# Kernel tuning notes

Measured on AMD Instinct MI355X. Metric: run time of the kernel, lower is better.

The kernel has to match this reference:

```python
import jax, jax.numpy as jnp
import numpy as np

NUM_SELECTS = 2
NOISE_EPS = 0.01
LOSS_COEF = 0.01
INV_SQRT2 = 0.7071067811865476


def _phi(z):
    # standard normal CDF
    return 0.5 * (1.0 + jax.lax.erf(z * INV_SQRT2))


def _cv_squared(v, eps=1e-10):
    # torch .var() uses unbiased estimator (ddof=1)
    return jnp.var(v, ddof=1) / (jnp.mean(v) ** 2 + eps)


def setup_inputs() -> dict:
    key = jax.random.key(0)
    ks = jax.random.split(key, 5)
    T, D, E = 8192, 4096, 16
    return {
        "x": jax.random.normal(ks[0], (T, D), jnp.float32),
        "gate_w1": jax.random.normal(ks[1], (E, D), jnp.float32) * 0.02,
        "gate_w2": jax.random.normal(ks[2], (E, E), jnp.float32) * 0.02,
        "noise_w": jax.random.normal(ks[3], (E, D), jnp.float32) * 0.02,
        "noise": jax.random.normal(ks[4], (T, E), jnp.float32),
    }


def reference(x, gate_w1, gate_w2, noise_w, noise):
    T = x.shape[0]
    # gate network: Linear -> tanh -> Linear (no biases)
    logits_gate = jnp.tanh(x @ gate_w1.T) @ gate_w2.T          # [T, E]
    noise_control = jax.nn.softplus(x @ noise_w.T) + NOISE_EPS  # [T, E]
    logits_noise = noise * noise_control                        # [T, E]
    logits = logits_gate + logits_noise

    # top (k+1) for load-balancing thresholds
    top_logits, top_indices = jax.lax.top_k(logits, NUM_SELECTS + 1)
    top_k_logits = top_logits[:, :NUM_SELECTS]
    top_k_indices = top_indices[:, :NUM_SELECTS]
    top_k_scores = jax.nn.softmax(top_k_logits, axis=1)

    # importance: scatter top-k scores back to [T, E]
    rows = jnp.arange(T)[:, None]
    scores_filtered = jnp.zeros_like(logits).at[rows, top_k_indices].set(top_k_scores)
    importance = scores_filtered.sum(0)  # [E]

    # load: prob each expert would be in the top-k under the noise model
    thr_in = top_logits[:, NUM_SELECTS][:, None]        # (k+1)-th largest
    thr_out = top_logits[:, NUM_SELECTS - 1][:, None]   # k-th largest
    is_in = logits_noise > thr_in
    prob_if_in = _phi((logits_gate - thr_in) / noise_control)
    prob_if_out = _phi((logits_gate - thr_out) / noise_control)
    load = jnp.where(is_in, prob_if_in, prob_if_out).sum(0)  # [E]

    gate_loss = (_cv_squared(importance) + _cv_squared(load)) * LOSS_COEF
    return top_k_indices, top_k_scores, gate_loss
```

## Files before the change

kernel.cpp:

```cpp
#include <hip/hip_runtime.h>
#include <math.h>

#define TT 8192
#define DD 4096

typedef float  f32x4  __attribute__((ext_vector_type(4)));
typedef short  bf16x8 __attribute__((ext_vector_type(8)));
typedef unsigned int u32;
typedef unsigned short u16;

__global__ __launch_bounds__(128)
void split_w(const float* __restrict__ gw1, const float* __restrict__ nw,
             u32* __restrict__ wfrag, float* __restrict__ iml) {
  const int s = blockIdx.x;
  const int t = threadIdx.x;
  if (s == 0 && t < 32) iml[t] = 0.f;
  const int h = t >> 6, l = t & 63;
  const int e = h * 16 + (l & 15);
  const float* src = ((e < 16) ? (gw1 + (size_t)e * DD) : (nw + (size_t)(e - 16) * DD))
                     + s * 32 + ((l >> 4) << 3);
  float f[8];
  *(float4*)&f[0] = *(const float4*)src;
  *(float4*)&f[4] = *(const float4*)(src + 4);
  u32 u0[8], u1[8], u2[8];
#pragma unroll
  for (int i = 0; i < 8; ++i) {
    u0[i] = __float_as_uint(f[i]);
    const float r1 = f[i] - __uint_as_float(u0[i] & 0xFFFF0000u);
    u1[i] = __float_as_uint(r1);
    const float r2 = r1 - __uint_as_float(u1[i] & 0xFFFF0000u);
    u2[i] = __float_as_uint(r2);
  }
  const size_t base = ((size_t)s * 2 + h) * 256 + l * 4;
#define PK(U) make_uint4((U[0]>>16)|(U[1]&0xFFFF0000u), (U[2]>>16)|(U[3]&0xFFFF0000u), \
                         (U[4]>>16)|(U[5]&0xFFFF0000u), (U[6]>>16)|(U[7]&0xFFFF0000u))
  *(uint4*)(wfrag + base)                 = PK(u0);
  *(uint4*)(wfrag + base + 128 * 512)     = PK(u1);
  *(uint4*)(wfrag + base + 2 * 128 * 512) = PK(u2);
#undef PK
}

__global__ __launch_bounds__(256)
void gate_gemm(const float* __restrict__ x, const u32* __restrict__ wfrag,
               float* __restrict__ part) {
  const int t = threadIdx.x;
  const int wt = blockIdx.x * 4 + (t >> 6);
  const int l = t & 63;
  const int rt = wt >> 3;
  const int ksl = wt & 7;
  const int r = l & 15, c = l >> 4;
  const float* xp = x + (size_t)(rt * 16 + r) * DD + ksl * 512 + (c << 3);
  const u32* wfl = wfrag + (size_t)l * 4;

  f32x4 ag0 = {0,0,0,0}, ag1 = ag0, ag2 = ag0, an0 = ag0, an1 = ag0, an2 = ag0;

#pragma unroll 4
  for (int sl = 0; sl < 16; ++sl) {
    float f[8];
    *(float4*)&f[0] = *(const float4*)(xp + sl * 32);
    *(float4*)&f[4] = *(const float4*)(xp + sl * 32 + 4);

    const int S = ksl * 16 + sl;
    const u32* wb = wfl + (size_t)S * 512;
    const bf16x8 bg0 = *(const bf16x8*)(wb);
    const bf16x8 bn0 = *(const bf16x8*)(wb + 256);
    const bf16x8 bg1 = *(const bf16x8*)(wb + 128 * 512);
    const bf16x8 bn1 = *(const bf16x8*)(wb + 128 * 512 + 256);
    const bf16x8 bg2 = *(const bf16x8*)(wb + 2 * 128 * 512);
    const bf16x8 bn2 = *(const bf16x8*)(wb + 2 * 128 * 512 + 256);

    u32 u0[8], u1[8], u2[8];
#pragma unroll
    for (int i = 0; i < 8; ++i) {
      u0[i] = __float_as_uint(f[i]);
      const float r1 = f[i] - __uint_as_float(u0[i] & 0xFFFF0000u);
      u1[i] = __float_as_uint(r1);
      const float r2 = r1 - __uint_as_float(u1[i] & 0xFFFF0000u);
      u2[i] = __float_as_uint(r2);
    }
    u32 pk[12];
#pragma unroll
    for (int i = 0; i < 4; ++i) {
      pk[i]     = (u0[2*i] >> 16) | (u0[2*i+1] & 0xFFFF0000u);
      pk[4 + i] = (u1[2*i] >> 16) | (u1[2*i+1] & 0xFFFF0000u);
      pk[8 + i] = (u2[2*i] >> 16) | (u2[2*i+1] & 0xFFFF0000u);
    }
    const bf16x8 a0 = *(const bf16x8*)&pk[0];
    const bf16x8 a1 = *(const bf16x8*)&pk[4];
    const bf16x8 a2 = *(const bf16x8*)&pk[8];

    ag0 = __builtin_amdgcn_mfma_f32_16x16x32_bf16(a0, bg0, ag0, 0, 0, 0);
    an0 = __builtin_amdgcn_mfma_f32_16x16x32_bf16(a0, bn0, an0, 0, 0, 0);
    ag1 = __builtin_amdgcn_mfma_f32_16x16x32_bf16(a0, bg1, ag1, 0, 0, 0);
    an1 = __builtin_amdgcn_mfma_f32_16x16x32_bf16(a0, bn1, an1, 0, 0, 0);
    ag2 = __builtin_amdgcn_mfma_f32_16x16x32_bf16(a1, bg0, ag2, 0, 0, 0);
    an2 = __builtin_amdgcn_mfma_f32_16x16x32_bf16(a1, bn0, an2, 0, 0, 0);
    ag0 = __builtin_amdgcn_mfma_f32_16x16x32_bf16(a0, bg2, ag0, 0, 0, 0);
    an0 = __builtin_amdgcn_mfma_f32_16x16x32_bf16(a0, bn2, an0, 0, 0, 0);
    ag1 = __builtin_amdgcn_mfma_f32_16x16x32_bf16(a1, bg1, ag1, 0, 0, 0);
    an1 = __builtin_amdgcn_mfma_f32_16x16x32_bf16(a1, bn1, an1, 0, 0, 0);
    ag2 = __builtin_amdgcn_mfma_f32_16x16x32_bf16(a2, bg0, ag2, 0, 0, 0);
    an2 = __builtin_amdgcn_mfma_f32_16x16x32_bf16(a2, bn0, an2, 0, 0, 0);
  }

  const f32x4 cg = ag0 + ag1 + ag2;
  const f32x4 cn = an0 + an1 + an2;
  const int e = l & 15;
  const int rbase = rt * 16 + ((l >> 4) << 2);
  *(f32x4*)&part[((size_t)(ksl * 32 + e)) * TT + rbase]      = cg;
  *(f32x4*)&part[((size_t)(ksl * 32 + 16 + e)) * TT + rbase] = cn;
}

__global__ __launch_bounds__(256)
void gate_epilogue(const float* __restrict__ part, const float* __restrict__ noise,
                   const float* __restrict__ gw2, float* __restrict__ out,
                   float* __restrict__ iml) {
  const int row = blockIdx.x * 256 + threadIdx.x;
  float dot[32];
#pragma unroll
  for (int e = 0; e < 32; ++e) {
    float s = 0.f;
#pragma unroll
    for (int sl = 0; sl < 8; ++sl) s += part[((size_t)(sl * 32 + e)) * TT + row];
    dot[e] = s;
  }
  float h[16];
#pragma unroll
  for (int e = 0; e < 16; ++e) h[e] = tanhf(dot[e]);
  float lg[16], nc[16], ln[16], l[16];
#pragma unroll
  for (int j = 0; j < 16; ++j) {
    float s = 0.f;
#pragma unroll
    for (int e = 0; e < 16; ++e) s = fmaf(h[e], gw2[j * 16 + e], s);
    lg[j] = s;
    const float v = dot[16 + j];
    nc[j] = fmaxf(v, 0.f) + log1pf(expf(-fabsf(v))) + 0.01f;
    ln[j] = noise[(size_t)row * 16 + j] * nc[j];
    l[j] = lg[j] + ln[j];
  }
  int i0 = 0; float m0 = l[0];
#pragma unroll
  for (int j = 1; j < 16; ++j) if (l[j] > m0) { m0 = l[j]; i0 = j; }
  int i1 = -1; float m1 = -1e30f;
#pragma unroll
  for (int j = 0; j < 16; ++j) if (j != i0 && l[j] > m1) { m1 = l[j]; i1 = j; }
  float m2 = -1e30f;
#pragma unroll
  for (int j = 0; j < 16; ++j) if (j != i0 && j != i1 && l[j] > m2) m2 = l[j];

  const float e1 = expf(m1 - m0);
  const float s0 = 1.f / (1.f + e1);
  const float s1 = e1 / (1.f + e1);
  out[(size_t)row * 2]             = (float)i0;
  out[(size_t)row * 2 + 1]         = (float)i1;
  out[16384 + (size_t)row * 2]     = s0;
  out[16384 + (size_t)row * 2 + 1] = s1;

  float c[32];
#pragma unroll
  for (int j = 0; j < 16; ++j) {
    c[j] = (j == i0) ? s0 : ((j == i1) ? s1 : 0.f);
    const bool in = ln[j] > m2;
    const float thr = in ? m2 : m1;
    const float z = (lg[j] - thr) / nc[j];
    c[16 + j] = 0.5f * (1.f + erff(z * 0.70710678118654752f));
  }
#pragma unroll
  for (int off = 32; off; off >>= 1) {
#pragma unroll
    for (int k = 0; k < 32; ++k) c[k] += __shfl_xor(c[k], off, 64);
  }
  __shared__ float sacc[32];
  if (threadIdx.x < 32) sacc[threadIdx.x] = 0.f;
  __syncthreads();
  if ((threadIdx.x & 63) == 0) {
#pragma unroll
    for (int k = 0; k < 32; ++k) atomicAdd(&sacc[k], c[k]);
  }
  __syncthreads();
  if (threadIdx.x < 32) atomicAdd(&iml[threadIdx.x], sacc[threadIdx.x]);
}

__global__ void gate_loss_k(const float* __restrict__ iml, float* __restrict__ out) {
  if (threadIdx.x == 0 && blockIdx.x == 0) {
    float res = 0.f;
    for (int g = 0; g < 2; ++g) {
      const float* v = iml + g * 16;
      float mu = 0.f;
      for (int j = 0; j < 16; ++j) mu += v[j];
      mu *= (1.f / 16.f);
      float var = 0.f;
      for (int j = 0; j < 16; ++j) { const float d = v[j] - mu; var += d * d; }
      var *= (1.f / 15.f);
      res += var / (mu * mu + 1e-10f);
    }
    out[32768] = res * 0.01f;
  }
}

extern "C" void kernel_launch(void* const* d_in, const int* in_sizes, int n_in,
                              void* d_out, int out_size, void* d_ws, size_t ws_size,
                              hipStream_t stream) {
  const float* x     = (const float*)d_in[0];
  const float* gw1   = (const float*)d_in[1];
  const float* gw2   = (const float*)d_in[2];
  const float* nw    = (const float*)d_in[3];
  const float* noise = (const float*)d_in[4];
  float* out  = (float*)d_out;
  float* part = (float*)d_ws;
  u32*   wfrag = (u32*)((char*)d_ws + (size_t)8 * 32 * TT * 4);
  float* iml  = (float*)((char*)d_ws + (size_t)8 * 32 * TT * 4 + (size_t)3 * 128 * 2 * 64 * 16);
  split_w<<<128, 128, 0, stream>>>(gw1, nw, wfrag, iml);
  gate_gemm<<<1024, 256, 0, stream>>>(x, wfrag, part);
  gate_epilogue<<<32, 256, 0, stream>>>(part, noise, gw2, out, iml);
  gate_loss_k<<<1, 64, 0, stream>>>(iml, out);
}
```

Measured before the change: 66.11 us.

## Fuse gate GEMM with epilogue and reduce partial sums in shared memory

Merges the split-K GEMM and the epilogue into one kernel. Each 512-thread block handles 16 rows with 8 waves, one per K slice, and sums the partials in LDS instead of writing an 8x32xT partial buffer to global memory and reading it back. Per-block importance and load sums go to a small buffer that the final loss kernel reduces deterministically, so the global atomics and the zeroing of iml in split_w are no longer needed. In exchange, only 16 of 512 threads run the epilogue math, which serialises that tail work inside each block.

```diff
diff --git a/kernel.cpp b/kernel.cpp
--- a/kernel.cpp
+++ b/kernel.cpp
@@ -7,14 +7,12 @@
 typedef float  f32x4  __attribute__((ext_vector_type(4)));
 typedef short  bf16x8 __attribute__((ext_vector_type(8)));
 typedef unsigned int u32;
-typedef unsigned short u16;
 
 __global__ __launch_bounds__(128)
 void split_w(const float* __restrict__ gw1, const float* __restrict__ nw,
-             u32* __restrict__ wfrag, float* __restrict__ iml) {
+             u32* __restrict__ wfrag) {
   const int s = blockIdx.x;
   const int t = threadIdx.x;
-  if (s == 0 && t < 32) iml[t] = 0.f;
   const int h = t >> 6, l = t & 63;
   const int e = h * 16 + (l & 15);
   const float* src = ((e < 16) ? (gw1 + (size_t)e * DD) : (nw + (size_t)(e - 16) * DD))
@@ -40,28 +38,30 @@
 #undef PK
 }
 
-__global__ __launch_bounds__(256)
-void gate_gemm(const float* __restrict__ x, const u32* __restrict__ wfrag,
-               float* __restrict__ part) {
+__global__ __launch_bounds__(512, 4)
+void gate_mega(const float* __restrict__ x, const u32* __restrict__ wfrag,
+               const float* __restrict__ noise, const float* __restrict__ gw2,
+               float* __restrict__ out, float* __restrict__ part2) {
+  __shared__ float red[8][512];
+  __shared__ float sg2[256];
   const int t = threadIdx.x;
-  const int wt = blockIdx.x * 4 + (t >> 6);
-  const int l = t & 63;
-  const int rt = wt >> 3;
-  const int ksl = wt & 7;
+  const int w = t >> 6, l = t & 63;
+  const int rt = blockIdx.x;
+  if (t < 256) sg2[t] = gw2[t];
+
   const int r = l & 15, c = l >> 4;
-  const float* xp = x + (size_t)(rt * 16 + r) * DD + ksl * 512 + (c << 3);
-  const u32* wfl = wfrag + (size_t)l * 4;
+  const float* xp = x + (size_t)(rt * 16 + r) * DD + w * 512 + (c << 3);
+  const u32* wfl = wfrag + (size_t)l * 4 + (size_t)(w * 16) * 512;
 
   f32x4 ag0 = {0,0,0,0}, ag1 = ag0, ag2 = ag0, an0 = ag0, an1 = ag0, an2 = ag0;
 
-#pragma unroll 4
+#pragma unroll 2
   for (int sl = 0; sl < 16; ++sl) {
     float f[8];
     *(float4*)&f[0] = *(const float4*)(xp + sl * 32);
     *(float4*)&f[4] = *(const float4*)(xp + sl * 32 + 4);
 
-    const int S = ksl * 16 + sl;
-    const u32* wb = wfl + (size_t)S * 512;
+    const u32* wb = wfl + (size_t)sl * 512;
     const bf16x8 bg0 = *(const bf16x8*)(wb);
     const bf16x8 bn0 = *(const bf16x8*)(wb + 256);
     const bf16x8 bg1 = *(const bf16x8*)(wb + 128 * 512);
@@ -69,21 +69,22 @@
     const bf16x8 bg2 = *(const bf16x8*)(wb + 2 * 128 * 512);
     const bf16x8 bn2 = *(const bf16x8*)(wb + 2 * 128 * 512 + 256);
 
-    u32 u0[8], u1[8], u2[8];
-#pragma unroll
-    for (int i = 0; i < 8; ++i) {
-      u0[i] = __float_as_uint(f[i]);
-      const float r1 = f[i] - __uint_as_float(u0[i] & 0xFFFF0000u);
-      u1[i] = __float_as_uint(r1);
-      const float r2 = r1 - __uint_as_float(u1[i] & 0xFFFF0000u);
-      u2[i] = __float_as_uint(r2);
-    }
-    u32 pk[12];
-#pragma unroll
-    for (int i = 0; i < 4; ++i) {
-      pk[i]     = (u0[2*i] >> 16) | (u0[2*i+1] & 0xFFFF0000u);
-      pk[4 + i] = (u1[2*i] >> 16) | (u1[2*i+1] & 0xFFFF0000u);
-      pk[8 + i] = (u2[2*i] >> 16) | (u2[2*i+1] & 0xFFFF0000u);
+    u32 pk[12] __attribute__((aligned(16)));
+#pragma unroll
+    for (int p = 0; p < 4; ++p) {
+      const u32  a  = __float_as_uint(f[2*p]);
+      const float ra1 = f[2*p] - __uint_as_float(a & 0xFFFF0000u);
+      const u32  a1 = __float_as_uint(ra1);
+      const float ra2 = ra1 - __uint_as_float(a1 & 0xFFFF0000u);
+      const u32  a2 = __float_as_uint(ra2);
+      const u32  b  = __float_as_uint(f[2*p+1]);
+      const float rb1 = f[2*p+1] - __uint_as_float(b & 0xFFFF0000u);
+      const u32  b1 = __float_as_uint(rb1);
+      const float rb2 = rb1 - __uint_as_float(b1 & 0xFFFF0000u);
+      const u32  b2 = __float_as_uint(rb2);
+      pk[p]     = (a  >> 16) | (b  & 0xFFFF0000u);
+      pk[4 + p] = (a1 >> 16) | (b1 & 0xFFFF0000u);
+      pk[8 + p] = (a2 >> 16) | (b2 & 0xFFFF0000u);
     }
     const bf16x8 a0 = *(const bf16x8*)&pk[0];
     const bf16x8 a1 = *(const bf16x8*)&pk[4];
@@ -105,93 +106,104 @@
 
   const f32x4 cg = ag0 + ag1 + ag2;
   const f32x4 cn = an0 + an1 + an2;
-  const int e = l & 15;
-  const int rbase = rt * 16 + ((l >> 4) << 2);
-  *(f32x4*)&part[((size_t)(ksl * 32 + e)) * TT + rbase]      = cg;
-  *(f32x4*)&part[((size_t)(ksl * 32 + 16 + e)) * TT + rbase] = cn;
+#pragma unroll
+  for (int j = 0; j < 4; ++j) {
+    red[w][r * 16 + (c * 4 + j)]        = cg[j];
+    red[w][(16 + r) * 16 + (c * 4 + j)] = cn[j];
+  }
+  __syncthreads();
+  {
+    float s = red[0][t];
+#pragma unroll
+    for (int ww = 1; ww < 8; ++ww) s += red[ww][t];
+    red[0][t] = s;
+  }
+  __syncthreads();
+
+  if (t < 16) {
+    const int row = rt * 16 + t;
+    float dot[32];
+#pragma unroll
+    for (int e = 0; e < 32; ++e) dot[e] = red[0][e * 16 + t];
+    float h[16];
+#pragma unroll
+    for (int e = 0; e < 16; ++e) h[e] = tanhf(dot[e]);
+    float lg[16], nc[16], ln[16], lo[16];
+#pragma unroll
+    for (int j = 0; j < 16; ++j) {
+      float s = 0.f;
+#pragma unroll
+      for (int e = 0; e < 16; ++e) s = fmaf(h[e], sg2[j * 16 + e], s);
+      lg[j] = s;
+      const float v = dot[16 + j];
+      nc[j] = fmaxf(v, 0.f) + log1pf(expf(-fabsf(v))) + 0.01f;
+      ln[j] = noise[(size_t)row * 16 + j] * nc[j];
+      lo[j] = lg[j] + ln[j];
+    }
+    int i0 = 0; float m0 = lo[0];
+#pragma unroll
+    for (int j = 1; j < 16; ++j) if (lo[j] > m0) { m0 = lo[j]; i0 = j; }
+    int i1 = -1; float m1 = -1e30f;
+#pragma unroll
+    for (int j = 0; j < 16; ++j) if (j != i0 && lo[j] > m1) { m1 = lo[j]; i1 = j; }
+    float m2 = -1e30f;
+#pragma unroll
+    for (int j = 0; j < 16; ++j) if (j != i0 && j != i1 && lo[j] > m2) m2 = lo[j];
+
+    const float e1 = expf(m1 - m0);
+    const float s0 = 1.f / (1.f + e1);
+    const float s1 = e1 / (1.f + e1);
+    out[(size_t)row * 2]             = (float)i0;
+    out[(size_t)row * 2 + 1]         = (float)i1;
+    out[16384 + (size_t)row * 2]     = s0;
+    out[16384 + (size_t)row * 2 + 1] = s1;
+
+    float cacc[32];
+#pragma unroll
+    for (int j = 0; j < 16; ++j) {
+      cacc[j] = (j == i0) ? s0 : ((j == i1) ? s1 : 0.f);
+      const bool in = ln[j] > m2;
+      const float thr = in ? m2 : m1;
+      const float z = (lg[j] - thr) / nc[j];
+      cacc[16 + j] = 0.5f * (1.f + erff(z * 0.70710678118654752f));
+    }
+#pragma unroll
+    for (int off = 1; off < 16; off <<= 1) {
+#pragma unroll
+      for (int k = 0; k < 32; ++k) cacc[k] += __shfl_xor(cacc[k], off, 16);
+    }
+    float v0 = 0.f, v1 = 0.f;
+#pragma unroll
+    for (int k = 0; k < 16; ++k) if (t == k) { v0 = cacc[k]; v1 = cacc[16 + k]; }
+    part2[(size_t)rt * 32 + t]      = v0;
+    part2[(size_t)rt * 32 + 16 + t] = v1;
+  }
 }
 
 __global__ __launch_bounds__(256)
-void gate_epilogue(const float* __restrict__ part, const float* __restrict__ noise,
-                   const float* __restrict__ gw2, float* __restrict__ out,
-                   float* __restrict__ iml) {
-  const int row = blockIdx.x * 256 + threadIdx.x;
-  float dot[32];
-#pragma unroll
-  for (int e = 0; e < 32; ++e) {
-    float s = 0.f;
-#pragma unroll
-    for (int sl = 0; sl < 8; ++sl) s += part[((size_t)(sl * 32 + e)) * TT + row];
-    dot[e] = s;
-  }
-  float h[16];
-#pragma unroll
-  for (int e = 0; e < 16; ++e) h[e] = tanhf(dot[e]);
-  float lg[16], nc[16], ln[16], l[16];
-#pragma unroll
-  for (int j = 0; j < 16; ++j) {
-    float s = 0.f;
-#pragma unroll
-    for (int e = 0; e < 16; ++e) s = fmaf(h[e], gw2[j * 16 + e], s);
-    lg[j] = s;
-    const float v = dot[16 + j];
-    nc[j] = fmaxf(v, 0.f) + log1pf(expf(-fabsf(v))) + 0.01f;
-    ln[j] = noise[(size_t)row * 16 + j] * nc[j];
-    l[j] = lg[j] + ln[j];
-  }
-  int i0 = 0; float m0 = l[0];
-#pragma unroll
-  for (int j = 1; j < 16; ++j) if (l[j] > m0) { m0 = l[j]; i0 = j; }
-  int i1 = -1; float m1 = -1e30f;
-#pragma unroll
-  for (int j = 0; j < 16; ++j) if (j != i0 && l[j] > m1) { m1 = l[j]; i1 = j; }
-  float m2 = -1e30f;
-#pragma unroll
-  for (int j = 0; j < 16; ++j) if (j != i0 && j != i1 && l[j] > m2) m2 = l[j];
-
-  const float e1 = expf(m1 - m0);
-  const float s0 = 1.f / (1.f + e1);
-  const float s1 = e1 / (1.f + e1);
-  out[(size_t)row * 2]             = (float)i0;
-  out[(size_t)row * 2 + 1]         = (float)i1;
-  out[16384 + (size_t)row * 2]     = s0;
-  out[16384 + (size_t)row * 2 + 1] = s1;
-
-  float c[32];
-#pragma unroll
-  for (int j = 0; j < 16; ++j) {
-    c[j] = (j == i0) ? s0 : ((j == i1) ? s1 : 0.f);
-    const bool in = ln[j] > m2;
-    const float thr = in ? m2 : m1;
-    const float z = (lg[j] - thr) / nc[j];
-    c[16 + j] = 0.5f * (1.f + erff(z * 0.70710678118654752f));
-  }
-#pragma unroll
-  for (int off = 32; off; off >>= 1) {
-#pragma unroll
-    for (int k = 0; k < 32; ++k) c[k] += __shfl_xor(c[k], off, 64);
-  }
-  __shared__ float sacc[32];
-  if (threadIdx.x < 32) sacc[threadIdx.x] = 0.f;
+void gate_loss_k(const float* __restrict__ part2, float* __restrict__ out) {
+  __shared__ float sred[8][32];
+  const int t = threadIdx.x;
+  const int k = t & 31, s = t >> 5;
+  float acc = 0.f;
+#pragma unroll 8
+  for (int i = 0; i < 64; ++i) acc += part2[(size_t)(s * 64 + i) * 32 + k];
+  sred[s][k] = acc;
   __syncthreads();
-  if ((threadIdx.x & 63) == 0) {
-#pragma unroll
-    for (int k = 0; k < 32; ++k) atomicAdd(&sacc[k], c[k]);
-  }
-  __syncthreads();
-  if (threadIdx.x < 32) atomicAdd(&iml[threadIdx.x], sacc[threadIdx.x]);
-}
-
-__global__ void gate_loss_k(const float* __restrict__ iml, float* __restrict__ out) {
-  if (threadIdx.x == 0 && blockIdx.x == 0) {
+  if (t == 0) {
     float res = 0.f;
     for (int g = 0; g < 2; ++g) {
-      const float* v = iml + g * 16;
+      float vals[16];
       float mu = 0.f;
-      for (int j = 0; j < 16; ++j) mu += v[j];
+      for (int j = 0; j < 16; ++j) {
+        float s2 = 0.f;
+        for (int ss = 0; ss < 8; ++ss) s2 += sred[ss][g * 16 + j];
+        vals[j] = s2;
+        mu += s2;
+      }
       mu *= (1.f / 16.f);
       float var = 0.f;
-      for (int j = 0; j < 16; ++j) { const float d = v[j] - mu; var += d * d; }
+      for (int j = 0; j < 16; ++j) { const float d = vals[j] - mu; var += d * d; }
       var *= (1.f / 15.f);
       res += var / (mu * mu + 1e-10f);
     }
@@ -207,12 +219,10 @@
   const float* gw2   = (const float*)d_in[2];
   const float* nw    = (const float*)d_in[3];
   const float* noise = (const float*)d_in[4];
-  float* out  = (float*)d_out;
-  float* part = (float*)d_ws;
-  u32*   wfrag = (u32*)((char*)d_ws + (size_t)8 * 32 * TT * 4);
-  float* iml  = (float*)((char*)d_ws + (size_t)8 * 32 * TT * 4 + (size_t)3 * 128 * 2 * 64 * 16);
-  split_w<<<128, 128, 0, stream>>>(gw1, nw, wfrag, iml);
-  gate_gemm<<<1024, 256, 0, stream>>>(x, wfrag, part);
-  gate_epilogue<<<32, 256, 0, stream>>>(part, noise, gw2, out, iml);
-  gate_loss_k<<<1, 64, 0, stream>>>(iml, out);
-}
+  float* out   = (float*)d_out;
+  u32*   wfrag = (u32*)d_ws;
+  float* part2 = (float*)((char*)d_ws + (size_t)768 * 1024);
+  split_w<<<128, 128, 0, stream>>>(gw1, nw, wfrag);
+  gate_mega<<<512, 512, 0, stream>>>(x, wfrag, noise, gw2, out, part2);
+  gate_loss_k<<<1, 256, 0, stream>>>(part2, out);
+}
```

Measured after the change: 61.23 us. 7.4% less time.
